# Optimization experiments

Hardware: AMD Instinct MI355X
Metric: run time of the kernel (lower is better)

The kernel has to match this reference:

```python
import jax, jax.numpy as jnp
import numpy as np

LAMBDA_ORTHO = 0.01
MARGIN = 1.0
T = 8
EPS = 1e-8


def setup_inputs() -> dict:
    key = jax.random.key(0)
    ks = jax.random.split(key, 6)
    B, D, K, N = 4096, 768, 64, 1024
    v = jax.random.normal(ks[0], (B, D), dtype=jnp.float32)
    vhat = jax.random.normal(ks[1], (B, D), dtype=jnp.float32)
    g = jax.random.uniform(ks[2], (B, K), dtype=jnp.float32)
    F = jax.random.normal(ks[3], (K, D), dtype=jnp.float32)
    negatives = jax.random.normal(ks[4], (N, D), dtype=jnp.float32)
    mask = jax.random.randint(ks[5], (B,), 0, 2, dtype=jnp.int32)
    return {"v": v, "vhat": vhat, "g": g, "F": F, "negatives": negatives, "mask": mask}


def _l2(u, w):
    # sqrt(clamp(||u-w||^2, 0) + 1e-8), reducing over last dim
    d2 = jnp.clip(jnp.sum((u - w) ** 2, axis=-1), 0.0)
    return jnp.sqrt(d2 + EPS)


def reference(v, vhat, g, F, negatives, mask):
    maskf = mask.astype(v.dtype)
    msum = jnp.clip(maskf.sum(), 1.0)

    true_d = _l2(vhat, v)  # [B]

    # ---- contrastive loss: vectorized over all N negatives (expansion form of L2) ----
    d2 = (jnp.sum(vhat ** 2, axis=1)[:, None]
          + jnp.sum(negatives ** 2, axis=1)[None, :]
          - 2.0 * vhat @ negatives.T)                      # [B, N]
    neg_d = jnp.sqrt(jnp.clip(d2, 0.0) + EPS)              # [B, N]
    Ju = jnp.mean(jnp.clip(1.0 + true_d[:, None] - neg_d, 0.0), axis=1)  # [B]
    Ju = (Ju * maskf).sum() / msum

    # ---- focal triplet loss: top-t SMALLEST g per row ----
    neg_vals, idx = jax.lax.top_k(-g, T)                   # smallest t, ascending in g
    g_tz = -neg_vals                                       # [B, T]
    F_t = F[idx]                                           # [B, T, D] gather
    g_t = g_tz / (g_tz.sum(axis=1, keepdims=True) + 1e-10)
    m_t = MARGIN * (1.0 - g_t) ** 2                        # [B, T]
    d_neg = _l2(vhat[:, None, :], F_t)                     # [B, T]
    Jt = jnp.mean(jnp.clip(m_t + true_d[:, None] - d_neg, 0.0), axis=1)  # [B]
    Jt = (Jt * maskf).sum() / msum

    # ---- orthogonality: ||F F^T - I||_F^2 ----
    gram = F @ F.T                                          # [K, K]
    ortho = LAMBDA_ORTHO * jnp.sum((gram - jnp.eye(gram.shape[0], dtype=gram.dtype)) ** 2)

    return Ju + Jt + ortho
```

## Files before the change

kernel.cpp:

```cpp
#include <hip/hip_runtime.h>
#include <math.h>

#define KD 768
#define T_SEL 8

typedef float f32x4v __attribute__((ext_vector_type(4)));
typedef __bf16 bf16x8 __attribute__((ext_vector_type(8)));

__device__ __forceinline__ float wave_sum(float x) {
#pragma unroll
  for (int o = 32; o > 0; o >>= 1) x += __shfl_xor(x, o, 64);
  return x;
}

__device__ __forceinline__ unsigned short f2bf(float x) {
  unsigned int u = __float_as_uint(x);
  unsigned int r = (u + 0x7fffu + ((u >> 16) & 1u)) >> 16;
  return (unsigned short)r;
}

__device__ __forceinline__ ushort4 cvt4(float4 a) {
  ushort4 us;
  us.x = f2bf(a.x); us.y = f2bf(a.y); us.z = f2bf(a.z); us.w = f2bf(a.w);
  return us;
}

__device__ __forceinline__ void async_copy16(void* lds, const void* g) {
  __builtin_amdgcn_global_load_lds(
      (const __attribute__((address_space(1))) unsigned int*)g,
      (__attribute__((address_space(3))) unsigned int*)lds, 16, 0, 0);
}

__global__ __launch_bounds__(256) void k_prep(
    const float* __restrict__ v, const float* __restrict__ vhat,
    const float* __restrict__ negs, const float* __restrict__ F,
    unsigned short* __restrict__ A_bf, unsigned short* __restrict__ B_bf,
    float* __restrict__ nv2, float* __restrict__ true_d,
    float* __restrict__ colBn) {
  const int w = threadIdx.x >> 6, l = threadIdx.x & 63;
  const int row = blockIdx.x * 4 + w;
  if (row < 4096) {
    const float4* vr = (const float4*)(vhat + (size_t)row * KD);
    const float4* vv = (const float4*)(v + (size_t)row * KD);
    ushort4* outb = (ushort4*)(A_bf + (size_t)row * KD);
    float s2 = 0.f, td2 = 0.f;
#pragma unroll
    for (int i = 0; i < 3; ++i) {
      float4 a = vr[i * 64 + l];
      float4 b = vv[i * 64 + l];
      s2 += a.x * a.x + a.y * a.y + a.z * a.z + a.w * a.w;
      float dx = a.x - b.x, dy = a.y - b.y, dz = a.z - b.z, dw = a.w - b.w;
      td2 += dx * dx + dy * dy + dz * dz + dw * dw;
      outb[i * 64 + l] = cvt4(a);
    }
    s2 = wave_sum(s2);
    td2 = wave_sum(td2);
    if (l == 0) {
      nv2[row] = s2;
      true_d[row] = sqrtf(fmaxf(td2, 0.f) + 1e-8f);
    }
  } else if (row < 5120) {
    const int r = row - 4096;
    const float4* nr = (const float4*)(negs + (size_t)r * KD);
    ushort4* outb = (ushort4*)(B_bf + (size_t)r * KD);
    float s2 = 0.f;
#pragma unroll
    for (int i = 0; i < 3; ++i) {
      float4 a = nr[i * 64 + l];
      s2 += a.x * a.x + a.y * a.y + a.z * a.z + a.w * a.w;
      outb[i * 64 + l] = cvt4(a);
    }
    s2 = wave_sum(s2);
    if (l == 0) colBn[r] = s2;
  } else if (row < 5184) {
    const int r = row - 5120;
    const float4* fr4 = (const float4*)(F + (size_t)r * KD);
    ushort4* ob1 = (ushort4*)(B_bf + (size_t)(1024 + r) * KD);
    ushort4* ob2 = (ushort4*)(A_bf + (size_t)(4096 + r) * KD);
    float s2 = 0.f;
#pragma unroll
    for (int i = 0; i < 3; ++i) {
      float4 a = fr4[i * 64 + l];
      s2 += a.x * a.x + a.y * a.y + a.z * a.z + a.w * a.w;
      ushort4 us = cvt4(a);
      ob1[i * 64 + l] = us;
      ob2[i * 64 + l] = us;
    }
    s2 = wave_sum(s2);
    if (l == 0) colBn[1024 + r] = s2;
  } else {
    const int r = row - 5184;
    ushort4* outb = (ushort4*)(A_bf + (size_t)(4160 + r) * KD);
    ushort4 z; z.x = 0; z.y = 0; z.z = 0; z.w = 0;
#pragma unroll
    for (int i = 0; i < 3; ++i) outb[i * 64 + l] = z;
  }
}

__global__ __launch_bounds__(256) void k_gemm(
    const unsigned short* __restrict__ Abf, const unsigned short* __restrict__ Bbf,
    const float* __restrict__ nv2, const float* __restrict__ colBn,
    const float* __restrict__ true_d, const int* __restrict__ mask,
    float* __restrict__ S, float* __restrict__ gemm_part, float* __restrict__ or_sum) {
  __shared__ char smem[24576];
  char* sA = smem;
  char* sB = smem + 16384;

  const int tid = threadIdx.x;
  const int w = tid >> 6;
  const int l = tid & 63;
  const int bid = blockIdx.x;
  const int tm = bid % 33;
  const int tn = bid / 33;

  if (tm == 32 && tn < 16) {
    if (tid == 0) gemm_part[bid] = 0.f;
    return;
  }

  const int row0 = tm * 128;
  const int col0 = tn * 64;
  const int wr = w >> 1, wc = w & 1;
  const int lr = l >> 3;
  const int sl = l & 7;

  f32x4v accf[4][2] = {};

  for (int kt = 0; kt < 12; ++kt) {
    const int k0 = kt * 64;
    if (kt) __syncthreads();
#pragma unroll
    for (int i = 0; i < 6; ++i) {
      const int c = w + i * 4;
      if (c < 16) {
        const int rr = c * 8 + lr;
        const int ss = sl ^ (rr & 7);
        async_copy16(sA + c * 1024, Abf + ((size_t)(row0 + rr) * KD + k0 + ss * 8));
      } else {
        const int cc = c - 16;
        const int rr = cc * 8 + lr;
        const int ss = sl ^ (rr & 7);
        async_copy16(sB + cc * 1024, Bbf + ((size_t)(col0 + rr) * KD + k0 + ss * 8));
      }
    }
    __syncthreads();

    const int fr = l & 15, fq = l >> 4;
#pragma unroll
    for (int kk = 0; kk < 2; ++kk) {
      bf16x8 af[4], bfr[2];
#pragma unroll
      for (int m = 0; m < 4; ++m) {
        const int rr = wr * 64 + m * 16 + fr;
        const int slot = (fq + kk * 4) ^ (rr & 7);
        af[m] = *(const bf16x8*)(sA + rr * 128 + slot * 16);
      }
#pragma unroll
      for (int n = 0; n < 2; ++n) {
        const int rr = wc * 32 + n * 16 + fr;
        const int slot = (fq + kk * 4) ^ (rr & 7);
        bfr[n] = *(const bf16x8*)(sB + rr * 128 + slot * 16);
      }
#pragma unroll
      for (int m = 0; m < 4; ++m)
#pragma unroll
        for (int n = 0; n < 2; ++n)
          accf[m][n] = __builtin_amdgcn_mfma_f32_16x16x32_bf16(af[m], bfr[n], accf[m][n], 0, 0, 0);
    }
  }

  const int fr = l & 15, fq = l >> 4;
  float local = 0.f;
  if (tm < 32 && tn < 16) {
#pragma unroll
    for (int m = 0; m < 4; ++m) {
#pragma unroll
      for (int j = 0; j < 4; ++j) {
        const int grow = row0 + wr * 64 + m * 16 + fq * 4 + j;
        const float nv = nv2[grow];
        const float td = true_d[grow];
        const float mf = (float)mask[grow];
#pragma unroll
        for (int n = 0; n < 2; ++n) {
          const int gcol = col0 + wc * 32 + n * 16 + fr;
          const float s = accf[m][n][j];
          const float d2 = nv + colBn[gcol] - 2.f * s;
          const float dn = sqrtf(fmaxf(d2, 0.f) + 1e-8f);
          local += mf * fmaxf(1.f + td - dn, 0.f);
        }
      }
    }
  } else if (tm < 32) {
#pragma unroll
    for (int m = 0; m < 4; ++m) {
#pragma unroll
      for (int j = 0; j < 4; ++j) {
        const int grow = row0 + wr * 64 + m * 16 + fq * 4 + j;
#pragma unroll
        for (int n = 0; n < 2; ++n) {
          const int gcol = col0 + wc * 32 + n * 16 + fr;
          S[(size_t)grow * 64 + (gcol - 1024)] = accf[m][n][j];
        }
      }
    }
  } else {
#pragma unroll
    for (int m = 0; m < 4; ++m) {
#pragma unroll
      for (int j = 0; j < 4; ++j) {
        const int grow = row0 + wr * 64 + m * 16 + fq * 4 + j;
        if (grow < 4160) {
          const int i2 = grow - 4096;
#pragma unroll
          for (int n = 0; n < 2; ++n) {
            const int gcol = col0 + wc * 32 + n * 16 + fr;
            const int j2 = gcol - 1024;
            const float d = accf[m][n][j] - ((i2 == j2) ? 1.f : 0.f);
            local += d * d;
          }
        }
      }
    }
  }

  local = wave_sum(local);
  __syncthreads();
  float* red = (float*)smem;
  if (l == 0) red[w] = local;
  __syncthreads();
  if (tid == 0) {
    const float t = red[0] + red[1] + red[2] + red[3];
    if (tm == 32) {
      or_sum[0] = t;
      gemm_part[bid] = 0.f;
    } else {
      gemm_part[bid] = (tn < 16) ? t : 0.f;
    }
  }
}

__global__ __launch_bounds__(256) void k_jt(
    const float* __restrict__ g, const float* __restrict__ S,
    const float* __restrict__ nv2, const float* __restrict__ true_d,
    const float* __restrict__ colBn, const int* __restrict__ mask,
    float* __restrict__ jt_part, float* __restrict__ ms_part) {
  const int w = threadIdx.x >> 6, l = threadIdx.x & 63;
  const int row = blockIdx.x * 4 + w;
  const float gl = g[(size_t)row * 64 + l];
  int rank = 0;
#pragma unroll
  for (int d = 1; d < 64; ++d) {
    const float o = __shfl_xor(gl, d, 64);
    const int j = l ^ d;
    rank += (o < gl || (o == gl && j < l)) ? 1 : 0;
  }
  const bool sel = rank < T_SEL;
  const float gsum = wave_sum(sel ? gl : 0.f) + 1e-10f;
  const float s = S[(size_t)row * 64 + l];
  const float d2 = nv2[row] + colBn[1024 + l] - 2.f * s;
  const float dneg = sqrtf(fmaxf(d2, 0.f) + 1e-8f);
  const float gt = gl / gsum;
  const float mt = (1.f - gt) * (1.f - gt);
  const float td = true_d[row];
  const float term = sel ? fmaxf(mt + td - dneg, 0.f) : 0.f;
  const float jt = wave_sum(term);
  const float mf = (float)mask[row];

  __shared__ float red[2][4];
  if (l == 0) {
    red[0][w] = jt * mf;
    red[1][w] = mf;
  }
  __syncthreads();
  if (threadIdx.x == 0) {
    jt_part[blockIdx.x] = red[0][0] + red[0][1] + red[0][2] + red[0][3];
    ms_part[blockIdx.x] = red[1][0] + red[1][1] + red[1][2] + red[1][3];
  }
}

__global__ __launch_bounds__(256) void k_final(
    const float* __restrict__ jt_part, const float* __restrict__ ms_part,
    const float* __restrict__ gemm_part, const float* __restrict__ or_sum,
    float* __restrict__ out) {
  const int tid = threadIdx.x;
  float sj = 0.f, sm = 0.f, su = 0.f;
  for (int i = tid; i < 1024; i += 256) {
    sj += jt_part[i];
    sm += ms_part[i];
  }
  for (int i = tid; i < 561; i += 256) su += gemm_part[i];
  sj = wave_sum(sj);
  sm = wave_sum(sm);
  su = wave_sum(su);
  __shared__ float r[3][4];
  const int w = tid >> 6, l = tid & 63;
  if (l == 0) { r[0][w] = sj; r[1][w] = sm; r[2][w] = su; }
  __syncthreads();
  if (tid == 0) {
    const float jt = r[0][0] + r[0][1] + r[0][2] + r[0][3];
    float ms = r[1][0] + r[1][1] + r[1][2] + r[1][3];
    const float ju = r[2][0] + r[2][1] + r[2][2] + r[2][3];
    ms = fmaxf(ms, 1.f);
    out[0] = ju / (1024.f * ms) + jt / (8.f * ms) + 0.01f * or_sum[0];
  }
}

extern "C" void kernel_launch(void* const* d_in, const int* in_sizes, int n_in,
                              void* d_out, int out_size, void* d_ws, size_t ws_size,
                              hipStream_t stream) {
  const float* v = (const float*)d_in[0];
  const float* vhat = (const float*)d_in[1];
  const float* g = (const float*)d_in[2];
  const float* F = (const float*)d_in[3];
  const float* negs = (const float*)d_in[4];
  const int* mask = (const int*)d_in[5];
  float* out = (float*)d_out;

  char* ws = (char*)d_ws;
  float* true_d = (float*)(ws + 0);
  float* nv2 = (float*)(ws + 16384);
  float* colBn = (float*)(ws + 32768);
  float* jt_part = (float*)(ws + 37120);
  float* ms_part = (float*)(ws + 41216);
  float* gemm_part = (float*)(ws + 45312);
  float* or_sum = (float*)(ws + 47616);
  float* S = (float*)(ws + 49152);
  unsigned short* A_bf = (unsigned short*)(ws + 1097728);
  unsigned short* B_bf = (unsigned short*)(ws + 7585792);

  hipLaunchKernelGGL(k_prep, dim3(1312), dim3(256), 0, stream, v, vhat, negs, F,
                     A_bf, B_bf, nv2, true_d, colBn);
  hipLaunchKernelGGL(k_gemm, dim3(561), dim3(256), 0, stream, A_bf, B_bf,
                     nv2, colBn, true_d, mask, S, gemm_part, or_sum);
  hipLaunchKernelGGL(k_jt, dim3(1024), dim3(256), 0, stream, g, S, nv2, true_d,
                     colBn, mask, jt_part, ms_part);
  hipLaunchKernelGGL(k_final, dim3(1), dim3(256), 0, stream, jt_part, ms_part,
                     gemm_part, or_sum, out);
}
```

Before: 108.1 us.

## Fuse focal triplet loss into GEMM epilogue and drop separate jt kernel

Moves the top-8 selection and g-sum into the prep kernel, where they are stored as a 64-bit selection mask and a per-row sum. The GEMM epilogue for the F columns then computes the triplet term directly instead of writing the S matrix. This removes the k_jt launch and the S round trip through memory. The grid is also reshaped to drop the empty tiles. k_final now recomputes the mask sum itself, and partial sums are pre-scaled in the GEMM.

Measured after the change: 119.8 us. 10.8% more time.

```diff
diff --git a/kernel.cpp b/kernel.cpp
--- a/kernel.cpp
+++ b/kernel.cpp
@@ -34,9 +34,11 @@
 __global__ __launch_bounds__(256) void k_prep(
     const float* __restrict__ v, const float* __restrict__ vhat,
     const float* __restrict__ negs, const float* __restrict__ F,
+    const float* __restrict__ g,
     unsigned short* __restrict__ A_bf, unsigned short* __restrict__ B_bf,
     float* __restrict__ nv2, float* __restrict__ true_d,
-    float* __restrict__ colBn) {
+    float* __restrict__ colBn, unsigned long long* __restrict__ selmask,
+    float* __restrict__ gsum) {
   const int w = threadIdx.x >> 6, l = threadIdx.x & 63;
   const int row = blockIdx.x * 4 + w;
   if (row < 4096) {
@@ -55,9 +57,22 @@
     }
     s2 = wave_sum(s2);
     td2 = wave_sum(td2);
+    const float gl = g[(size_t)row * 64 + l];
+    int rank = 0;
+#pragma unroll
+    for (int d = 1; d < 64; ++d) {
+      const float o = __shfl_xor(gl, d, 64);
+      const int j = l ^ d;
+      rank += (o < gl || (o == gl && j < l)) ? 1 : 0;
+    }
+    const bool sel = rank < T_SEL;
+    const float gs = wave_sum(sel ? gl : 0.f) + 1e-10f;
+    const unsigned long long sm = __ballot(sel);
     if (l == 0) {
       nv2[row] = s2;
       true_d[row] = sqrtf(fmaxf(td2, 0.f) + 1e-8f);
+      selmask[row] = sm;
+      gsum[row] = gs;
     }
   } else if (row < 5120) {
     const int r = row - 4096;
@@ -101,7 +116,9 @@
     const unsigned short* __restrict__ Abf, const unsigned short* __restrict__ Bbf,
     const float* __restrict__ nv2, const float* __restrict__ colBn,
     const float* __restrict__ true_d, const int* __restrict__ mask,
-    float* __restrict__ S, float* __restrict__ gemm_part, float* __restrict__ or_sum) {
+    const float* __restrict__ g, const unsigned long long* __restrict__ selmask,
+    const float* __restrict__ gsum,
+    float* __restrict__ gemm_part, float* __restrict__ or_sum) {
   __shared__ char smem[24576];
   char* sA = smem;
   char* sB = smem + 16384;
@@ -110,13 +127,8 @@
   const int w = tid >> 6;
   const int l = tid & 63;
   const int bid = blockIdx.x;
-  const int tm = bid % 33;
-  const int tn = bid / 33;
-
-  if (tm == 32 && tn < 16) {
-    if (tid == 0) gemm_part[bid] = 0.f;
-    return;
-  }
+  const int tm = (bid == 544) ? 32 : (bid & 31);
+  const int tn = (bid == 544) ? 16 : (bid >> 5);
 
   const int row0 = tm * 128;
   const int col0 = tn * 64;
@@ -171,7 +183,7 @@
 
   const int fr = l & 15, fq = l >> 4;
   float local = 0.f;
-  if (tm < 32 && tn < 16) {
+  if (tn < 16) {
 #pragma unroll
     for (int m = 0; m < 4; ++m) {
 #pragma unroll
@@ -190,19 +202,33 @@
         }
       }
     }
+    local *= (1.f / 1024.f);
   } else if (tm < 32) {
 #pragma unroll
     for (int m = 0; m < 4; ++m) {
 #pragma unroll
       for (int j = 0; j < 4; ++j) {
         const int grow = row0 + wr * 64 + m * 16 + fq * 4 + j;
+        const float nv = nv2[grow];
+        const float td = true_d[grow];
+        const float mf = (float)mask[grow];
+        const float gs = gsum[grow];
+        const unsigned long long msk = selmask[grow];
 #pragma unroll
         for (int n = 0; n < 2; ++n) {
-          const int gcol = col0 + wc * 32 + n * 16 + fr;
-          S[(size_t)grow * 64 + (gcol - 1024)] = accf[m][n][j];
+          const int k = wc * 32 + n * 16 + fr;
+          if ((msk >> k) & 1ull) {
+            const float s = accf[m][n][j];
+            const float d2 = nv + colBn[1024 + k] - 2.f * s;
+            const float dn = sqrtf(fmaxf(d2, 0.f) + 1e-8f);
+            const float gt = g[(size_t)grow * 64 + k] / gs;
+            const float mt = (1.f - gt) * (1.f - gt);
+            local += mf * fmaxf(mt + td - dn, 0.f);
+          }
         }
       }
     }
+    local *= (1.f / (float)T_SEL);
   } else {
 #pragma unroll
     for (int m = 0; m < 4; ++m) {
@@ -213,8 +239,7 @@
           const int i2 = grow - 4096;
 #pragma unroll
           for (int n = 0; n < 2; ++n) {
-            const int gcol = col0 + wc * 32 + n * 16 + fr;
-            const int j2 = gcol - 1024;
+            const int j2 = wc * 32 + n * 16 + fr;
             const float d = accf[m][n][j] - ((i2 == j2) ? 1.f : 0.f);
             local += d * d;
           }
@@ -230,78 +255,28 @@
   __syncthreads();
   if (tid == 0) {
     const float t = red[0] + red[1] + red[2] + red[3];
-    if (tm == 32) {
-      or_sum[0] = t;
-      gemm_part[bid] = 0.f;
-    } else {
-      gemm_part[bid] = (tn < 16) ? t : 0.f;
-    }
-  }
-}
-
-__global__ __launch_bounds__(256) void k_jt(
-    const float* __restrict__ g, const float* __restrict__ S,
-    const float* __restrict__ nv2, const float* __restrict__ true_d,
-    const float* __restrict__ colBn, const int* __restrict__ mask,
-    float* __restrict__ jt_part, float* __restrict__ ms_part) {
-  const int w = threadIdx.x >> 6, l = threadIdx.x & 63;
-  const int row = blockIdx.x * 4 + w;
-  const float gl = g[(size_t)row * 64 + l];
-  int rank = 0;
-#pragma unroll
-  for (int d = 1; d < 64; ++d) {
-    const float o = __shfl_xor(gl, d, 64);
-    const int j = l ^ d;
-    rank += (o < gl || (o == gl && j < l)) ? 1 : 0;
-  }
-  const bool sel = rank < T_SEL;
-  const float gsum = wave_sum(sel ? gl : 0.f) + 1e-10f;
-  const float s = S[(size_t)row * 64 + l];
-  const float d2 = nv2[row] + colBn[1024 + l] - 2.f * s;
-  const float dneg = sqrtf(fmaxf(d2, 0.f) + 1e-8f);
-  const float gt = gl / gsum;
-  const float mt = (1.f - gt) * (1.f - gt);
-  const float td = true_d[row];
-  const float term = sel ? fmaxf(mt + td - dneg, 0.f) : 0.f;
-  const float jt = wave_sum(term);
-  const float mf = (float)mask[row];
-
-  __shared__ float red[2][4];
-  if (l == 0) {
-    red[0][w] = jt * mf;
-    red[1][w] = mf;
-  }
-  __syncthreads();
-  if (threadIdx.x == 0) {
-    jt_part[blockIdx.x] = red[0][0] + red[0][1] + red[0][2] + red[0][3];
-    ms_part[blockIdx.x] = red[1][0] + red[1][1] + red[1][2] + red[1][3];
+    if (bid == 544) or_sum[0] = t;
+    else gemm_part[bid] = t;
   }
 }
 
 __global__ __launch_bounds__(256) void k_final(
-    const float* __restrict__ jt_part, const float* __restrict__ ms_part,
     const float* __restrict__ gemm_part, const float* __restrict__ or_sum,
-    float* __restrict__ out) {
+    const int* __restrict__ mask, float* __restrict__ out) {
   const int tid = threadIdx.x;
-  float sj = 0.f, sm = 0.f, su = 0.f;
-  for (int i = tid; i < 1024; i += 256) {
-    sj += jt_part[i];
-    sm += ms_part[i];
-  }
-  for (int i = tid; i < 561; i += 256) su += gemm_part[i];
-  sj = wave_sum(sj);
+  float sp = 0.f, sm = 0.f;
+  for (int i = tid; i < 544; i += 256) sp += gemm_part[i];
+  for (int i = tid; i < 4096; i += 256) sm += (float)mask[i];
+  sp = wave_sum(sp);
   sm = wave_sum(sm);
-  su = wave_sum(su);
-  __shared__ float r[3][4];
+  __shared__ float r[2][4];
   const int w = tid >> 6, l = tid & 63;
-  if (l == 0) { r[0][w] = sj; r[1][w] = sm; r[2][w] = su; }
+  if (l == 0) { r[0][w] = sp; r[1][w] = sm; }
   __syncthreads();
   if (tid == 0) {
-    const float jt = r[0][0] + r[0][1] + r[0][2] + r[0][3];
-    float ms = r[1][0] + r[1][1] + r[1][2] + r[1][3];
-    const float ju = r[2][0] + r[2][1] + r[2][2] + r[2][3];
-    ms = fmaxf(ms, 1.f);
-    out[0] = ju / (1024.f * ms) + jt / (8.f * ms) + 0.01f * or_sum[0];
+    const float parts = r[0][0] + r[0][1] + r[0][2] + r[0][3];
+    const float msum = fmaxf(r[1][0] + r[1][1] + r[1][2] + r[1][3], 1.f);
+    out[0] = parts / msum + 0.01f * or_sum[0];
   }
 }
 
@@ -320,20 +295,16 @@
   float* true_d = (float*)(ws + 0);
   float* nv2 = (float*)(ws + 16384);
   float* colBn = (float*)(ws + 32768);
-  float* jt_part = (float*)(ws + 37120);
-  float* ms_part = (float*)(ws + 41216);
-  float* gemm_part = (float*)(ws + 45312);
-  float* or_sum = (float*)(ws + 47616);
-  float* S = (float*)(ws + 49152);
-  unsigned short* A_bf = (unsigned short*)(ws + 1097728);
-  unsigned short* B_bf = (unsigned short*)(ws + 7585792);
-
-  hipLaunchKernelGGL(k_prep, dim3(1312), dim3(256), 0, stream, v, vhat, negs, F,
-                     A_bf, B_bf, nv2, true_d, colBn);
-  hipLaunchKernelGGL(k_gemm, dim3(561), dim3(256), 0, stream, A_bf, B_bf,
-                     nv2, colBn, true_d, mask, S, gemm_part, or_sum);
-  hipLaunchKernelGGL(k_jt, dim3(1024), dim3(256), 0, stream, g, S, nv2, true_d,
-                     colBn, mask, jt_part, ms_part);
-  hipLaunchKernelGGL(k_final, dim3(1), dim3(256), 0, stream, jt_part, ms_part,
-                     gemm_part, or_sum, out);
-}
+  float* gsum = (float*)(ws + 40960);
+  unsigned long long* selmask = (unsigned long long*)(ws + 57344);
+  float* gemm_part = (float*)(ws + 90112);
+  float* or_sum = (float*)(ws + 94208);
+  unsigned short* A_bf = (unsigned short*)(ws + 98304);
+  unsigned short* B_bf = (unsigned short*)(ws + 6586368);
+
+  hipLaunchKernelGGL(k_prep, dim3(1312), dim3(256), 0, stream, v, vhat, negs, F, g,
+                     A_bf, B_bf, nv2, true_d, colBn, selmask, gsum);
+  hipLaunchKernelGGL(k_gemm, dim3(545), dim3(256), 0, stream, A_bf, B_bf,
+                     nv2, colBn, true_d, mask, g, selmask, gsum, gemm_part, or_sum);
+  hipLaunchKernelGGL(k_final, dim3(1), dim3(256), 0, stream, gemm_part, or_sum, mask, out);
+}
```

## Double-buffer LDS tiles in GEMM kernel and drop idle grid blocks

Applied to the files above, without the earlier changes.

The GEMM main loop now uses two LDS buffers. It issues the async copy for the next K tile before running the MFMAs on the current one, so global loads overlap with compute, and it needs one barrier per iteration instead of two. The block-index mapping is changed so the 16 blocks that used to exit immediately are never launched, and the final reduction reads 544 partials. LDS per block doubles to 48 KB, which may lower occupancy.

Result: faster. 102.5 us (-5.2%).

```diff
diff --git a/kernel.cpp b/kernel.cpp
--- a/kernel.cpp
+++ b/kernel.cpp
@@ -102,21 +102,16 @@
     const float* __restrict__ nv2, const float* __restrict__ colBn,
     const float* __restrict__ true_d, const int* __restrict__ mask,
     float* __restrict__ S, float* __restrict__ gemm_part, float* __restrict__ or_sum) {
-  __shared__ char smem[24576];
-  char* sA = smem;
-  char* sB = smem + 16384;
+  __shared__ char smem[49152];
 
   const int tid = threadIdx.x;
   const int w = tid >> 6;
   const int l = tid & 63;
   const int bid = blockIdx.x;
-  const int tm = bid % 33;
-  const int tn = bid / 33;
-
-  if (tm == 32 && tn < 16) {
-    if (tid == 0) gemm_part[bid] = 0.f;
-    return;
-  }
+  int tm, tn;
+  if (bid < 512) { tm = bid & 31; tn = bid >> 5; }
+  else if (bid < 544) { tm = bid - 512; tn = 16; }
+  else { tm = 32; tn = 16; }
 
   const int row0 = tm * 128;
   const int col0 = tn * 64;
@@ -126,26 +121,34 @@
 
   f32x4v accf[4][2] = {};
 
+#define STAGE(p, kt)                                                                   \
+  {                                                                                    \
+    char* sA_ = smem + (p)*24576;                                                      \
+    char* sB_ = sA_ + 16384;                                                           \
+    const int k0_ = (kt)*64;                                                           \
+    _Pragma("unroll") for (int i = 0; i < 6; ++i) {                                    \
+      const int c = w + i * 4;                                                         \
+      if (c < 16) {                                                                    \
+        const int rr = c * 8 + lr;                                                     \
+        const int ss = sl ^ (rr & 7);                                                  \
+        async_copy16(sA_ + c * 1024, Abf + ((size_t)(row0 + rr) * KD + k0_ + ss * 8)); \
+      } else {                                                                         \
+        const int cc = c - 16;                                                         \
+        const int rr = cc * 8 + lr;                                                    \
+        const int ss = sl ^ (rr & 7);                                                  \
+        async_copy16(sB_ + cc * 1024, Bbf + ((size_t)(col0 + rr) * KD + k0_ + ss * 8));\
+      }                                                                                \
+    }                                                                                  \
+  }
+
+  const int fr = l & 15, fq = l >> 4;
+  STAGE(0, 0);
+  __syncthreads();
+  int cur = 0;
   for (int kt = 0; kt < 12; ++kt) {
-    const int k0 = kt * 64;
-    if (kt) __syncthreads();
-#pragma unroll
-    for (int i = 0; i < 6; ++i) {
-      const int c = w + i * 4;
-      if (c < 16) {
-        const int rr = c * 8 + lr;
-        const int ss = sl ^ (rr & 7);
-        async_copy16(sA + c * 1024, Abf + ((size_t)(row0 + rr) * KD + k0 + ss * 8));
-      } else {
-        const int cc = c - 16;
-        const int rr = cc * 8 + lr;
-        const int ss = sl ^ (rr & 7);
-        async_copy16(sB + cc * 1024, Bbf + ((size_t)(col0 + rr) * KD + k0 + ss * 8));
-      }
-    }
-    __syncthreads();
-
-    const int fr = l & 15, fq = l >> 4;
+    if (kt + 1 < 12) STAGE(cur ^ 1, kt + 1);
+    char* sA = smem + cur * 24576;
+    char* sB = sA + 16384;
 #pragma unroll
     for (int kk = 0; kk < 2; ++kk) {
       bf16x8 af[4], bfr[2];
@@ -167,11 +170,13 @@
         for (int n = 0; n < 2; ++n)
           accf[m][n] = __builtin_amdgcn_mfma_f32_16x16x32_bf16(af[m], bfr[n], accf[m][n], 0, 0, 0);
     }
-  }
-
-  const int fr = l & 15, fq = l >> 4;
+    __syncthreads();
+    cur ^= 1;
+  }
+#undef STAGE
+
   float local = 0.f;
-  if (tm < 32 && tn < 16) {
+  if (tn < 16) {
 #pragma unroll
     for (int m = 0; m < 4; ++m) {
 #pragma unroll
@@ -213,8 +218,7 @@
           const int i2 = grow - 4096;
 #pragma unroll
           for (int n = 0; n < 2; ++n) {
-            const int gcol = col0 + wc * 32 + n * 16 + fr;
-            const int j2 = gcol - 1024;
+            const int j2 = wc * 32 + n * 16 + fr;
             const float d = accf[m][n][j] - ((i2 == j2) ? 1.f : 0.f);
             local += d * d;
           }
@@ -230,12 +234,8 @@
   __syncthreads();
   if (tid == 0) {
     const float t = red[0] + red[1] + red[2] + red[3];
-    if (tm == 32) {
-      or_sum[0] = t;
-      gemm_part[bid] = 0.f;
-    } else {
-      gemm_part[bid] = (tn < 16) ? t : 0.f;
-    }
+    if (bid == 544) or_sum[0] = t;
+    else gemm_part[bid] = t;
   }
 }
 
@@ -288,7 +288,7 @@
     sj += jt_part[i];
     sm += ms_part[i];
   }
-  for (int i = tid; i < 561; i += 256) su += gemm_part[i];
+  for (int i = tid; i < 544; i += 256) su += gemm_part[i];
   sj = wave_sum(sj);
   sm = wave_sum(sm);
   su = wave_sum(su);
@@ -330,7 +330,7 @@
 
   hipLaunchKernelGGL(k_prep, dim3(1312), dim3(256), 0, stream, v, vhat, negs, F,
                      A_bf, B_bf, nv2, true_d, colBn);
-  hipLaunchKernelGGL(k_gemm, dim3(561), dim3(256), 0, stream, A_bf, B_bf,
+  hipLaunchKernelGGL(k_gemm, dim3(545), dim3(256), 0, stream, A_bf, B_bf,
                      nv2, colBn, true_d, mask, S, gemm_part, or_sum);
   hipLaunchKernelGGL(k_jt, dim3(1024), dim3(256), 0, stream, g, S, nv2, true_d,
                      colBn, mask, jt_part, ms_part);
```
